# Optimization experiments

Hardware: AMD Instinct MI355X
Metric: run time of the kernel (lower is better)

## Reference

```python
import jax, jax.numpy as jnp
import numpy as np

SOFTMAX_TEMP = 0.01
CART_PIXEL_WIDTH = 256
CART_RESOLUTION = 0.2592


def zn_desc(desc):
    # desc: B x C x N. Zero-mean, unit-std over channel dim (torch.std default ddof=1).
    mean = jnp.mean(desc, axis=1, keepdims=True)
    std = jnp.std(desc, axis=1, keepdims=True, ddof=1)
    return (desc - mean) / std


def compute_2D_from_3D(coords):
    cart_min_range = (CART_PIXEL_WIDTH / 2 - 0.5) * CART_RESOLUTION
    u = (cart_min_range + coords[:, 1]) / CART_RESOLUTION
    v = (cart_min_range - coords[:, 0]) / CART_RESOLUTION
    return jnp.stack([u, v], axis=2)


def setup_inputs() -> dict:
    key = jax.random.key(0)
    B, C, N, H, W = 2, 256, 1024, 256, 256
    ks = jax.random.split(key, 4)
    tgt_coords = jax.random.normal(ks[0], (B, 3, H * W), jnp.float32) * 10.0
    tgt_weights = jax.random.uniform(ks[1], (B, 1, H, W), dtype=jnp.float32)
    src_desc_norm = zn_desc(jax.random.normal(ks[2], (B, C, N), jnp.float32))
    tgt_desc = jax.random.normal(ks[3], (B, C, H, W), jnp.float32)
    return {
        'geometry_img': jnp.zeros((1,), jnp.int32),
        'tgt_coords': tgt_coords,
        'tgt_2D': jnp.zeros((1,), jnp.int32),
        'tgt_weights': tgt_weights,
        'tgt_weights_dense': jnp.zeros((1,), jnp.int32),
        'src_desc_norm': src_desc_norm,
        'tgt_desc': tgt_desc,
        'tgt_desc_dense': jnp.zeros((1,), jnp.int32),
        'cam_calib': jnp.zeros((1,), jnp.int32),
        'window_size': 16,
    }


def reference(geometry_img, tgt_coords, tgt_2D, tgt_weights, tgt_weights_dense,
              src_desc_norm, tgt_desc, tgt_desc_dense, cam_calib, window_size):
    B, C = tgt_desc.shape[0], tgt_desc.shape[1]
    M = tgt_desc.shape[2] * tgt_desc.shape[3]
    N = src_desc_norm.shape[2]

    tgt_desc_flat = tgt_desc.reshape(B, C, M)
    tgt_desc_norm = zn_desc(tgt_desc_flat)

    # B x N x M similarity (ZNCC): src^T @ tgt / C
    match_vals = jnp.einsum('bcn,bcm->bnm', src_desc_norm, tgt_desc_norm) / float(C)
    soft_match_vals = jax.nn.softmax(match_vals / SOFTMAX_TEMP, axis=2)
    max_softmax = jnp.max(soft_match_vals, axis=(1, 2))  # (B,)

    # three weighted sums sharing the same softmax matrix
    pseudo_coords = jnp.einsum('bcm,bnm->bcn', tgt_coords, soft_match_vals)
    pseudo_weights = jnp.einsum('bcm,bnm->bcn', tgt_weights.reshape(B, 1, M), soft_match_vals)
    pseudo_descs = jnp.einsum('bcm,bnm->bcn', tgt_desc_flat, soft_match_vals)          # B x C x N

    pseudo_2D = compute_2D_from_3D(pseudo_coords)  # B x N x 2
    pseudo_descs = zn_desc(pseudo_descs)
    valid_pts = jnp.ones((B, 1, N), jnp.int32)
    return pseudo_coords, pseudo_weights, pseudo_descs, pseudo_2D, valid_pts, max_softmax
```

## Files before the change

### kernel.cpp

```cpp
#include <hip/hip_runtime.h>
#include <hip/hip_bf16.h>

#define Bb   2
#define Cc   256
#define Nn   1024
#define Mm   65536
#define MCn  16
#define VROWS 272
#define MSTEP 32
#define MCHUNK (Mm / MCn)
#define NIT  (MCHUNK / MSTEP)

#define SCL_OFF  0L
#define TMC_OFF  524288L
#define TCM_OFF  67633152L
#define SNC_OFF  138936320L
#define PART_OFF 139984896L
#define ZP_OFF   157810688L
#define PP_OFF   157941760L
#define PS_OFF   PART_OFF
#define PS2_OFF  (PART_OFF + 2097152L)

#define O_COORD 0L
#define O_W     6144L
#define O_DESC  8192L
#define O_P2D   532480L
#define O_VALID 536576L
#define O_MAXSM 538624L

using f32x4 = __attribute__((ext_vector_type(4))) float;
using s16x8 = __attribute__((ext_vector_type(8))) short;

__device__ inline unsigned short f2bf(float x) {
    union { float f; unsigned int u; } v; v.f = x;
    unsigned int r = v.u + 0x7FFFu + ((v.u >> 16) & 1u);
    return (unsigned short)(r >> 16);
}
__device__ inline float bf2f(unsigned short u) {
    union { unsigned int u; float f; } v; v.u = ((unsigned int)u) << 16;
    return v.f;
}
__device__ inline float exp2v(float x) {
    float r; asm("v_exp_f32 %0, %1" : "=v"(r) : "v"(x)); return r;
}
__device__ inline unsigned int cvtpk(float lo, float hi) {
    unsigned int r;
    asm("v_cvt_pk_bf16_f32 %0, %1, %2" : "=v"(r) : "v"(lo), "v"(hi));
    return r;
}

__device__ inline void gld_lds16(const unsigned short* g, unsigned short* l) {
    __builtin_amdgcn_global_load_lds(
        (const __attribute__((address_space(1))) unsigned int*)g,
        (__attribute__((address_space(3))) unsigned int*)l, 16, 0, 0);
}

__global__ void k_prep_tgt(const float* __restrict__ tgt,
                           unsigned short* __restrict__ tmc,
                           unsigned short* __restrict__ tcm,
                           float* __restrict__ ps,
                           float* __restrict__ ps2) {
    __shared__ float lds[64][65];
    __shared__ float sm[4][64], sm2[4][64];
    int b = blockIdx.z, cy = blockIdx.y, c0 = cy * 64;
    long m0 = (long)blockIdx.x * 64;
    int ty = threadIdx.x >> 6, tx = threadIdx.x & 63;
    float s = 0.f, s2 = 0.f;
    #pragma unroll
    for (int k = 0; k < 16; ++k) {
        int ci = 4 * k + ty;
        float v = tgt[((long)b * Cc + c0 + ci) * Mm + m0 + tx];
        lds[ci][tx] = v;
        s += v; s2 += v * v;
        tcm[((long)b * VROWS + c0 + ci) * Mm + m0 + tx] = f2bf(v);
    }
    sm[ty][tx] = s; sm2[ty][tx] = s2;
    __syncthreads();
    #pragma unroll
    for (int k = 0; k < 16; ++k) {
        int mi = 4 * k + ty;
        tmc[((long)b * Mm + m0 + mi) * Cc + c0 + tx] = f2bf(lds[tx][mi]);
    }
    if (ty == 0) {
        long o = ((long)b * 4 + cy) * Mm + m0 + tx;
        ps[o]  = (sm[0][tx] + sm[1][tx]) + (sm[2][tx] + sm[3][tx]);
        ps2[o] = (sm2[0][tx] + sm2[1][tx]) + (sm2[2][tx] + sm2[3][tx]);
    }
}

__global__ void k_stats(const float* __restrict__ ps,
                        const float* __restrict__ ps2,
                        const float* __restrict__ coords,
                        const float* __restrict__ weights,
                        float* __restrict__ scl,
                        unsigned short* __restrict__ tcm) {
    int b = blockIdx.y;
    long m = (long)blockIdx.x * 256 + threadIdx.x;
    float s = 0.f, s2 = 0.f;
    #pragma unroll
    for (int k = 0; k < 4; ++k) {
        long o = ((long)b * 4 + k) * Mm + m;
        s += ps[o]; s2 += ps2[o];
    }
    float var = fmaxf((s2 - s * s * (1.0f / Cc)) * (1.0f / (Cc - 1)), 1e-20f);
    scl[(long)b * Mm + m] = 1.4426950408889634f * rsqrtf(var) * (1.0f / (Cc * 0.01f));
    unsigned short* vrow = tcm + ((long)b * VROWS + 256) * Mm + m;
    #pragma unroll
    for (int i = 0; i < 3; ++i) vrow[(long)i * Mm] = f2bf(coords[((long)b * 3 + i) * Mm + m]);
    vrow[3L * Mm] = f2bf(weights[(long)b * Mm + m]);
    vrow[4L * Mm] = 0x3F80;
    #pragma unroll
    for (int i = 5; i < 16; ++i) vrow[(long)i * Mm] = 0;
}

__global__ void k_prep_src(const float* __restrict__ src, unsigned short* __restrict__ snc) {
    __shared__ float lds[64][65];
    int b = blockIdx.z, c0 = blockIdx.y * 64, n0 = blockIdx.x * 64;
    int ty = threadIdx.x >> 6, tx = threadIdx.x & 63;
    #pragma unroll
    for (int k = 0; k < 16; ++k)
        lds[4 * k + ty][tx] = src[((long)b * Cc + c0 + 4 * k + ty) * Nn + n0 + tx];
    __syncthreads();
    #pragma unroll
    for (int k = 0; k < 16; ++k) {
        int ni = 4 * k + ty;
        snc[((long)b * Nn + n0 + ni) * Cc + c0 + tx] = f2bf(lds[tx][ni]);
    }
}

__global__ __launch_bounds__(256, 1) void k_main(const unsigned short* __restrict__ tmc,
                                                 const unsigned short* __restrict__ tcm,
                                                 const unsigned short* __restrict__ snc,
                                                 const float* __restrict__ scl,
                                                 unsigned short* __restrict__ part,
                                                 float* __restrict__ zp,
                                                 float* __restrict__ pp) {
    __shared__ __align__(16) unsigned short kb0[8192], kb1[8192];
    __shared__ __align__(16) unsigned short vb0[8704], vb1[8704];
    __shared__ __align__(16) unsigned short pbuf[4][2][16][56];

    int w = threadIdx.x >> 6, lane = threadIdx.x & 63;
    int l15 = lane & 15, lg = lane >> 4;
    int b = blockIdx.z, nt = blockIdx.y, mc = blockIdx.x;
    int nb = nt * 128 + w * 32;
    long mbase = (long)mc * MCHUNK;

    s16x8 qf[2][8];
    #pragma unroll
    for (int st = 0; st < 2; ++st) {
        const unsigned short* qp = snc + ((long)b * Nn + nb + st * 16 + l15) * Cc + lg * 8;
        #pragma unroll
        for (int cc = 0; cc < 8; ++cc) qf[st][cc] = *(const s16x8*)(qp + cc * 32);
    }

    f32x4 acc[2][17];
    #pragma unroll
    for (int st = 0; st < 2; ++st)
        #pragma unroll
        for (int t = 0; t < 17; ++t) acc[st][t] = (f32x4){0.f, 0.f, 0.f, 0.f};
    float pmax[2] = {0.f, 0.f};

    const unsigned short* tmcb = tmc + (long)b * Mm * Cc;
    const unsigned short* tcmb = tcm + (long)b * VROWS * (long)Mm;
    const unsigned short* ksrc[4];
    #pragma unroll
    for (int i = 0; i < 4; ++i) {
        int ins = w * 4 + i;
        int row = 2 * ins + (lane >> 5);
        int gs  = (lane & 31) ^ (row & 7);
        ksrc[i] = tmcb + (mbase + row) * Cc + gs * 8;
    }
    const unsigned short* vsrc[5];
    int vj = ((lane & 3) ^ ((lane >> 3) & 3)) * 8;
    #pragma unroll
    for (int i = 0; i < 5; ++i) {
        int ins = (i < 4) ? (w * 4 + i) : 16;
        int row = ins * 16 + (lane >> 2);
        vsrc[i] = tcmb + (long)row * Mm + mbase + vj;
    }

    const float* sclb = scl + (long)b * Mm;

    auto stage = [&](int d) {
        unsigned short* kd = d ? kb1 : kb0;
        unsigned short* vd = d ? vb1 : vb0;
        #pragma unroll
        for (int i = 0; i < 4; ++i) gld_lds16(ksrc[i], kd + (w * 4 + i) * 512);
        #pragma unroll
        for (int i = 0; i < 4; ++i) gld_lds16(vsrc[i], vd + (w * 4 + i) * 512);
        if (w == 3) gld_lds16(vsrc[4], vd + 16 * 512);
    };
    auto advance = [&]() {
        #pragma unroll
        for (int i = 0; i < 4; ++i) ksrc[i] += MSTEP * Cc;
        #pragma unroll
        for (int i = 0; i < 5; ++i) vsrc[i] += MSTEP;
    };

    stage(0);
    advance();
    __syncthreads();

    int ksw = (l15 & 7) << 3;
    int vsw = (lg ^ ((l15 >> 1) & 3)) * 8;

    float4 scA = *(const float4*)(sclb + mbase + lg * 4);
    float4 scB = *(const float4*)(sclb + mbase + 16 + lg * 4);

    for (int s = 0; s < NIT; ++s) {
        int cur = s & 1;
        if (s + 1 < NIT) { stage(cur ^ 1); advance(); }
        const unsigned short* kbc = cur ? kb1 : kb0;
        const unsigned short* vbc = cur ? vb1 : vb0;
        int sn = (s + 1 < NIT) ? s + 1 : s;
        float4 nA = *(const float4*)(sclb + mbase + (long)sn * MSTEP + lg * 4);
        float4 nB = *(const float4*)(sclb + mbase + (long)sn * MSTEP + 16 + lg * 4);

        #pragma unroll
        for (int t = 0; t < 2; ++t) {
            f32x4 dA = (f32x4){0.f, 0.f, 0.f, 0.f};
            f32x4 dB = (f32x4){0.f, 0.f, 0.f, 0.f};
            const unsigned short* kr = kbc + (t * 16 + l15) * Cc;
            #pragma unroll
            for (int cc = 0; cc < 8; ++cc) {
                s16x8 kf = *(const s16x8*)(kr + ((cc * 32 + lg * 8) ^ ksw));
                dA = __builtin_amdgcn_mfma_f32_16x16x32_bf16(kf, qf[0][cc], dA, 0, 0, 0);
                dB = __builtin_amdgcn_mfma_f32_16x16x32_bf16(kf, qf[1][cc], dB, 0, 0, 0);
            }
            float4 sc = t ? scB : scA;
            #pragma unroll
            for (int st = 0; st < 2; ++st) {
                f32x4 d = st ? dB : dA;
                float p0 = exp2v(d.x * sc.x);
                float p1 = exp2v(d.y * sc.y);
                float p2 = exp2v(d.z * sc.z);
                float p3 = exp2v(d.w * sc.w);
                pmax[st] = fmaxf(pmax[st], fmaxf(fmaxf(p0, p1), fmaxf(p2, p3)));
                unsigned long long pk =
                    (unsigned long long)cvtpk(p0, p1) | ((unsigned long long)cvtpk(p2, p3) << 32);
                *(unsigned long long*)&pbuf[w][st][l15][t * 16 + lg * 4] = pk;
            }
        }
        s16x8 pfA = *(const s16x8*)&pbuf[w][0][l15][lg * 8];
        s16x8 pfB = *(const s16x8*)&pbuf[w][1][l15][lg * 8];
        #pragma unroll
        for (int t = 0; t < 17; ++t) {
            s16x8 vf = *(const s16x8*)(vbc + (t * 16 + l15) * MSTEP + vsw);
            acc[0][t] = __builtin_amdgcn_mfma_f32_16x16x32_bf16(vf, pfA, acc[0][t], 0, 0, 0);
            acc[1][t] = __builtin_amdgcn_mfma_f32_16x16x32_bf16(vf, pfB, acc[1][t], 0, 0, 0);
        }
        scA = nA; scB = nB;
        __syncthreads();
    }

    #pragma unroll
    for (int st = 0; st < 2; ++st) {
        float pt = fmaxf(pmax[st], __shfl_xor(pmax[st], 16));
        pt = fmaxf(pt, __shfl_xor(pt, 32));
        long zi = ((long)(b * MCn + mc)) * Nn + nb + st * 16;
        if (lg == 1) zp[zi + l15] = acc[st][16].x;
        if (lane < 16) pp[zi + lane] = pt;
        unsigned short* po = part + (((long)(b * MCn + mc) * Nn) + nb + st * 16 + l15) * VROWS;
        #pragma unroll
        for (int t = 0; t < 17; ++t) {
            f32x4 a = acc[st][t];
            unsigned long long pk =
                (unsigned long long)cvtpk(a.x, a.y) | ((unsigned long long)cvtpk(a.z, a.w) << 32);
            *(unsigned long long*)&po[t * 16 + lg * 4] = pk;
        }
    }
}

__global__ void k_epi(const unsigned short* __restrict__ part,
                      const float* __restrict__ zp,
                      const float* __restrict__ pp,
                      float* __restrict__ out) {
    int w = threadIdx.x >> 6, lane = threadIdx.x & 63;
    int bn = blockIdx.x * 4 + w;
    int b = bn >> 10, n = bn & 1023;

    float Z = 0.f, pm = 0.f;
    #pragma unroll
    for (int mc = 0; mc < MCn; ++mc) {
        long zi = ((long)(b * MCn + mc)) * Nn + n;
        Z += zp[zi];
        pm = fmaxf(pm, pp[zi]);
    }
    float invZ = 1.0f / Z;

    float dv[4], s1 = 0.f, s2 = 0.f;
    #pragma unroll
    for (int k = 0; k < 4; ++k) {
        int c = lane + 64 * k;
        float s = 0.f;
        #pragma unroll
        for (int mc = 0; mc < MCn; ++mc)
            s += bf2f(part[((long)(b * MCn + mc) * Nn + n) * VROWS + c]);
        float d = s * invZ;
        dv[k] = d; s1 += d; s2 += d * d;
    }
    #pragma unroll
    for (int off = 1; off < 64; off <<= 1) { s1 += __shfl_xor(s1, off); s2 += __shfl_xor(s2, off); }
    float mean = s1 * (1.0f / 256.0f);
    float var = fmaxf((s2 - 256.0f * mean * mean) * (1.0f / 255.0f), 1e-20f);
    float istd = 1.0f / sqrtf(var);
    #pragma unroll
    for (int k = 0; k < 4; ++k)
        out[O_DESC + ((long)b * Cc + lane + 64 * k) * Nn + n] = (dv[k] - mean) * istd;

    float ex = 0.f;
    if (lane < 4) {
        int c = 256 + lane;
        #pragma unroll
        for (int mc = 0; mc < MCn; ++mc)
            ex += bf2f(part[((long)(b * MCn + mc) * Nn + n) * VROWS + c]);
        ex *= invZ;
    }
    float pc0 = __shfl(ex, 0), pc1 = __shfl(ex, 1), pc2 = __shfl(ex, 2), wv = __shfl(ex, 3);
    if (lane == 0) {
        out[O_COORD + ((long)b * 3 + 0) * Nn + n] = pc0;
        out[O_COORD + ((long)b * 3 + 1) * Nn + n] = pc1;
        out[O_COORD + ((long)b * 3 + 2) * Nn + n] = pc2;
        out[O_W + (long)b * Nn + n] = wv;
        const float cmin = 33.048f;
        out[O_P2D + ((long)b * Nn + n) * 2 + 0] = (cmin + pc1) * (1.0f / 0.2592f);
        out[O_P2D + ((long)b * Nn + n) * 2 + 1] = (cmin - pc0) * (1.0f / 0.2592f);
        out[O_VALID + (long)b * Nn + n] = 1.0f;
        atomicMax((unsigned int*)out + O_MAXSM + b, __float_as_uint(pm * invZ));
    }
}

extern "C" void kernel_launch(void* const* d_in, const int* in_sizes, int n_in,
                              void* d_out, int out_size, void* d_ws, size_t ws_size,
                              hipStream_t stream) {
    const float* tgt_coords  = (const float*)d_in[1];
    const float* tgt_weights = (const float*)d_in[3];
    const float* src_desc    = (const float*)d_in[5];
    const float* tgt_desc    = (const float*)d_in[6];

    char* ws = (char*)d_ws;
    float* scl           = (float*)(ws + SCL_OFF);
    unsigned short* tmc  = (unsigned short*)(ws + TMC_OFF);
    unsigned short* tcm  = (unsigned short*)(ws + TCM_OFF);
    unsigned short* snc  = (unsigned short*)(ws + SNC_OFF);
    unsigned short* part = (unsigned short*)(ws + PART_OFF);
    float* ps            = (float*)(ws + PS_OFF);
    float* ps2           = (float*)(ws + PS2_OFF);
    float* zp            = (float*)(ws + ZP_OFF);
    float* pp            = (float*)(ws + PP_OFF);
    float* out           = (float*)d_out;

    k_prep_tgt<<<dim3(Mm / 64, Cc / 64, Bb), 256, 0, stream>>>(tgt_desc, tmc, tcm, ps, ps2);
    k_stats<<<dim3(Mm / 256, Bb), 256, 0, stream>>>(ps, ps2, tgt_coords, tgt_weights, scl, tcm);
    k_prep_src<<<dim3(Nn / 64, Cc / 64, Bb), 256, 0, stream>>>(src_desc, snc);
    k_main<<<dim3(MCn, Nn / 128, Bb), 256, 0, stream>>>(tmc, tcm, snc, scl, part, zp, pp);
    hipMemsetAsync((char*)d_out + O_MAXSM * 4, 0, 2 * sizeof(float), stream);
    k_epi<<<dim3((Bb * Nn) / 4), 256, 0, stream>>>(part, zp, pp, out);
}
```

Before: 336.6 us.

## Widen per-wave N tile to 64 rows and split M into 32 chunks

Each wave now handles 64 source rows (4 MFMA sub-tiles) instead of 32, so each staged K/V tile in LDS feeds twice as many MFMAs and global/LDS traffic per unit of work is halved. To keep the grid size up, the M dimension is split into 32 chunks when the workspace is large enough, with the chunk count passed at runtime to the main and epilogue kernels. Accumulator registers double (4x17 f32x4), which may cause spills or lower occupancy. The epilogue reduction loop is no longer unrolled and now reads twice as many partials. The prefetch of the next scale values into registers is removed.

```diff
diff --git a/kernel.cpp b/kernel.cpp
--- a/kernel.cpp
+++ b/kernel.cpp
@@ -5,19 +5,14 @@
 #define Cc   256
 #define Nn   1024
 #define Mm   65536
-#define MCn  16
 #define VROWS 272
 #define MSTEP 32
-#define MCHUNK (Mm / MCn)
-#define NIT  (MCHUNK / MSTEP)
 
 #define SCL_OFF  0L
 #define TMC_OFF  524288L
 #define TCM_OFF  67633152L
 #define SNC_OFF  138936320L
 #define PART_OFF 139984896L
-#define ZP_OFF   157810688L
-#define PP_OFF   157941760L
 #define PS_OFF   PART_OFF
 #define PS2_OFF  (PART_OFF + 2097152L)
 
@@ -134,31 +129,34 @@
                                                  const float* __restrict__ scl,
                                                  unsigned short* __restrict__ part,
                                                  float* __restrict__ zp,
-                                                 float* __restrict__ pp) {
-    __shared__ __align__(16) unsigned short kb0[8192], kb1[8192];
-    __shared__ __align__(16) unsigned short vb0[8704], vb1[8704];
-    __shared__ __align__(16) unsigned short pbuf[4][2][16][56];
+                                                 float* __restrict__ pp,
+                                                 int mcn) {
+    __shared__ __align__(16) unsigned short kb[2][8192];
+    __shared__ __align__(16) unsigned short vb[2][8704];
+    __shared__ __align__(16) unsigned short pbuf[4][4][16][40];
 
     int w = threadIdx.x >> 6, lane = threadIdx.x & 63;
     int l15 = lane & 15, lg = lane >> 4;
     int b = blockIdx.z, nt = blockIdx.y, mc = blockIdx.x;
-    int nb = nt * 128 + w * 32;
-    long mbase = (long)mc * MCHUNK;
-
-    s16x8 qf[2][8];
-    #pragma unroll
-    for (int st = 0; st < 2; ++st) {
+    int nb = nt * 256 + w * 64;
+    int mchunk = Mm / mcn;
+    int nit = mchunk / MSTEP;
+    long mbase = (long)mc * mchunk;
+
+    s16x8 qf[4][8];
+    #pragma unroll
+    for (int st = 0; st < 4; ++st) {
         const unsigned short* qp = snc + ((long)b * Nn + nb + st * 16 + l15) * Cc + lg * 8;
         #pragma unroll
         for (int cc = 0; cc < 8; ++cc) qf[st][cc] = *(const s16x8*)(qp + cc * 32);
     }
 
-    f32x4 acc[2][17];
-    #pragma unroll
-    for (int st = 0; st < 2; ++st)
+    f32x4 acc[4][17];
+    #pragma unroll
+    for (int st = 0; st < 4; ++st)
         #pragma unroll
         for (int t = 0; t < 17; ++t) acc[st][t] = (f32x4){0.f, 0.f, 0.f, 0.f};
-    float pmax[2] = {0.f, 0.f};
+    float pmax[4] = {0.f, 0.f, 0.f, 0.f};
 
     const unsigned short* tmcb = tmc + (long)b * Mm * Cc;
     const unsigned short* tcmb = tcm + (long)b * VROWS * (long)Mm;
@@ -182,55 +180,53 @@
     const float* sclb = scl + (long)b * Mm;
 
     auto stage = [&](int d) {
-        unsigned short* kd = d ? kb1 : kb0;
-        unsigned short* vd = d ? vb1 : vb0;
+        unsigned short* kd = kb[d];
+        unsigned short* vd = vb[d];
         #pragma unroll
         for (int i = 0; i < 4; ++i) gld_lds16(ksrc[i], kd + (w * 4 + i) * 512);
         #pragma unroll
         for (int i = 0; i < 4; ++i) gld_lds16(vsrc[i], vd + (w * 4 + i) * 512);
         if (w == 3) gld_lds16(vsrc[4], vd + 16 * 512);
-    };
-    auto advance = [&]() {
         #pragma unroll
         for (int i = 0; i < 4; ++i) ksrc[i] += MSTEP * Cc;
         #pragma unroll
         for (int i = 0; i < 5; ++i) vsrc[i] += MSTEP;
     };
 
-    stage(0);
-    advance();
-    __syncthreads();
-
     int ksw = (l15 & 7) << 3;
     int vsw = (lg ^ ((l15 >> 1) & 3)) * 8;
 
-    float4 scA = *(const float4*)(sclb + mbase + lg * 4);
-    float4 scB = *(const float4*)(sclb + mbase + 16 + lg * 4);
-
-    for (int s = 0; s < NIT; ++s) {
+    stage(0);
+    __syncthreads();
+
+    for (int s = 0; s < nit; ++s) {
         int cur = s & 1;
-        if (s + 1 < NIT) { stage(cur ^ 1); advance(); }
-        const unsigned short* kbc = cur ? kb1 : kb0;
-        const unsigned short* vbc = cur ? vb1 : vb0;
-        int sn = (s + 1 < NIT) ? s + 1 : s;
-        float4 nA = *(const float4*)(sclb + mbase + (long)sn * MSTEP + lg * 4);
-        float4 nB = *(const float4*)(sclb + mbase + (long)sn * MSTEP + 16 + lg * 4);
+        if (s + 1 < nit) stage(cur ^ 1);
+        const unsigned short* kbc = kb[cur];
+        const unsigned short* vbc = vb[cur];
+        long m0 = mbase + (long)s * MSTEP;
+        float4 sc0 = *(const float4*)(sclb + m0 + lg * 4);
+        float4 sc1 = *(const float4*)(sclb + m0 + 16 + lg * 4);
 
         #pragma unroll
         for (int t = 0; t < 2; ++t) {
             f32x4 dA = (f32x4){0.f, 0.f, 0.f, 0.f};
             f32x4 dB = (f32x4){0.f, 0.f, 0.f, 0.f};
+            f32x4 dC = (f32x4){0.f, 0.f, 0.f, 0.f};
+            f32x4 dD = (f32x4){0.f, 0.f, 0.f, 0.f};
             const unsigned short* kr = kbc + (t * 16 + l15) * Cc;
             #pragma unroll
             for (int cc = 0; cc < 8; ++cc) {
                 s16x8 kf = *(const s16x8*)(kr + ((cc * 32 + lg * 8) ^ ksw));
                 dA = __builtin_amdgcn_mfma_f32_16x16x32_bf16(kf, qf[0][cc], dA, 0, 0, 0);
                 dB = __builtin_amdgcn_mfma_f32_16x16x32_bf16(kf, qf[1][cc], dB, 0, 0, 0);
+                dC = __builtin_amdgcn_mfma_f32_16x16x32_bf16(kf, qf[2][cc], dC, 0, 0, 0);
+                dD = __builtin_amdgcn_mfma_f32_16x16x32_bf16(kf, qf[3][cc], dD, 0, 0, 0);
             }
-            float4 sc = t ? scB : scA;
+            float4 sc = t ? sc1 : sc0;
             #pragma unroll
-            for (int st = 0; st < 2; ++st) {
-                f32x4 d = st ? dB : dA;
+            for (int st = 0; st < 4; ++st) {
+                f32x4 d = (st == 0) ? dA : (st == 1) ? dB : (st == 2) ? dC : dD;
                 float p0 = exp2v(d.x * sc.x);
                 float p1 = exp2v(d.y * sc.y);
                 float p2 = exp2v(d.z * sc.z);
@@ -243,24 +239,27 @@
         }
         s16x8 pfA = *(const s16x8*)&pbuf[w][0][l15][lg * 8];
         s16x8 pfB = *(const s16x8*)&pbuf[w][1][l15][lg * 8];
+        s16x8 pfC = *(const s16x8*)&pbuf[w][2][l15][lg * 8];
+        s16x8 pfD = *(const s16x8*)&pbuf[w][3][l15][lg * 8];
         #pragma unroll
         for (int t = 0; t < 17; ++t) {
             s16x8 vf = *(const s16x8*)(vbc + (t * 16 + l15) * MSTEP + vsw);
             acc[0][t] = __builtin_amdgcn_mfma_f32_16x16x32_bf16(vf, pfA, acc[0][t], 0, 0, 0);
             acc[1][t] = __builtin_amdgcn_mfma_f32_16x16x32_bf16(vf, pfB, acc[1][t], 0, 0, 0);
+            acc[2][t] = __builtin_amdgcn_mfma_f32_16x16x32_bf16(vf, pfC, acc[2][t], 0, 0, 0);
+            acc[3][t] = __builtin_amdgcn_mfma_f32_16x16x32_bf16(vf, pfD, acc[3][t], 0, 0, 0);
         }
-        scA = nA; scB = nB;
         __syncthreads();
     }
 
     #pragma unroll
-    for (int st = 0; st < 2; ++st) {
+    for (int st = 0; st < 4; ++st) {
         float pt = fmaxf(pmax[st], __shfl_xor(pmax[st], 16));
         pt = fmaxf(pt, __shfl_xor(pt, 32));
-        long zi = ((long)(b * MCn + mc)) * Nn + nb + st * 16;
+        long zi = ((long)(b * mcn + mc)) * Nn + nb + st * 16;
         if (lg == 1) zp[zi + l15] = acc[st][16].x;
         if (lane < 16) pp[zi + lane] = pt;
-        unsigned short* po = part + (((long)(b * MCn + mc) * Nn) + nb + st * 16 + l15) * VROWS;
+        unsigned short* po = part + (((long)(b * mcn + mc) * Nn) + nb + st * 16 + l15) * VROWS;
         #pragma unroll
         for (int t = 0; t < 17; ++t) {
             f32x4 a = acc[st][t];
@@ -274,15 +273,15 @@
 __global__ void k_epi(const unsigned short* __restrict__ part,
                       const float* __restrict__ zp,
                       const float* __restrict__ pp,
-                      float* __restrict__ out) {
+                      float* __restrict__ out,
+                      int mcn) {
     int w = threadIdx.x >> 6, lane = threadIdx.x & 63;
     int bn = blockIdx.x * 4 + w;
     int b = bn >> 10, n = bn & 1023;
 
     float Z = 0.f, pm = 0.f;
-    #pragma unroll
-    for (int mc = 0; mc < MCn; ++mc) {
-        long zi = ((long)(b * MCn + mc)) * Nn + n;
+    for (int mc = 0; mc < mcn; ++mc) {
+        long zi = ((long)(b * mcn + mc)) * Nn + n;
         Z += zp[zi];
         pm = fmaxf(pm, pp[zi]);
     }
@@ -293,9 +292,8 @@
     for (int k = 0; k < 4; ++k) {
         int c = lane + 64 * k;
         float s = 0.f;
-        #pragma unroll
-        for (int mc = 0; mc < MCn; ++mc)
-            s += bf2f(part[((long)(b * MCn + mc) * Nn + n) * VROWS + c]);
+        for (int mc = 0; mc < mcn; ++mc)
+            s += bf2f(part[((long)(b * mcn + mc) * Nn + n) * VROWS + c]);
         float d = s * invZ;
         dv[k] = d; s1 += d; s2 += d * d;
     }
@@ -311,9 +309,8 @@
     float ex = 0.f;
     if (lane < 4) {
         int c = 256 + lane;
-        #pragma unroll
-        for (int mc = 0; mc < MCn; ++mc)
-            ex += bf2f(part[((long)(b * MCn + mc) * Nn + n) * VROWS + c]);
+        for (int mc = 0; mc < mcn; ++mc)
+            ex += bf2f(part[((long)(b * mcn + mc) * Nn + n) * VROWS + c]);
         ex *= invZ;
     }
     float pc0 = __shfl(ex, 0), pc1 = __shfl(ex, 1), pc2 = __shfl(ex, 2), wv = __shfl(ex, 3);
@@ -346,14 +343,19 @@
     unsigned short* part = (unsigned short*)(ws + PART_OFF);
     float* ps            = (float*)(ws + PS_OFF);
     float* ps2           = (float*)(ws + PS2_OFF);
-    float* zp            = (float*)(ws + ZP_OFF);
-    float* pp            = (float*)(ws + PP_OFF);
     float* out           = (float*)d_out;
+
+    long need32 = PART_OFF + (long)Bb * 32 * Nn * VROWS * 2 + 2L * Bb * 32 * Nn * 4;
+    int mcn = (ws_size >= (size_t)need32) ? 32 : 16;
+    long zp_off = PART_OFF + (long)Bb * mcn * Nn * VROWS * 2;
+    long pp_off = zp_off + (long)Bb * mcn * Nn * 4;
+    float* zp = (float*)(ws + zp_off);
+    float* pp = (float*)(ws + pp_off);
 
     k_prep_tgt<<<dim3(Mm / 64, Cc / 64, Bb), 256, 0, stream>>>(tgt_desc, tmc, tcm, ps, ps2);
     k_stats<<<dim3(Mm / 256, Bb), 256, 0, stream>>>(ps, ps2, tgt_coords, tgt_weights, scl, tcm);
     k_prep_src<<<dim3(Nn / 64, Cc / 64, Bb), 256, 0, stream>>>(src_desc, snc);
-    k_main<<<dim3(MCn, Nn / 128, Bb), 256, 0, stream>>>(tmc, tcm, snc, scl, part, zp, pp);
-    hipMemsetAsync((char*)d_out + O_MAXSM * 4, 0, 2 * sizeof(float), stream);
-    k_epi<<<dim3((Bb * Nn) / 4), 256, 0, stream>>>(part, zp, pp, out);
-}
+    k_main<<<dim3(mcn, Nn / 256, Bb), 256, 0, stream>>>(tmc, tcm, snc, scl, part, zp, pp, mcn);
+    (void)hipMemsetAsync((char*)d_out + O_MAXSM * 4, 0, 2 * sizeof(float), stream);
+    k_epi<<<dim3((Bb * Nn) / 4), 256, 0, stream>>>(part, zp, pp, out, mcn);
+}
```

New measurement: 327.3 us. 1.03x faster.
